# Kernel optimization log

Hardware: AMD Instinct MI355X
Metric: run time of the kernel (lower is better)

Reference implementation:

```python
import jax, jax.numpy as jnp
import numpy as np
import math

B, S, D, H = 2, 2048, 2048, 16
HD = D // H  # head_dim = 128
NEG = -9e15


def setup_inputs() -> dict:
    key = jax.random.key(0)
    k1, k2, k3 = jax.random.split(key, 3)
    x = jax.random.normal(k1, (B, S, D), dtype=jnp.float32)
    Wqkv = jax.random.normal(k2, (D, 3 * D), dtype=jnp.float32) * (1.0 / math.sqrt(D))
    bqkv = jnp.zeros((3 * D,), dtype=jnp.float32)
    Wo = jax.random.normal(k3, (D, D), dtype=jnp.float32) * (1.0 / math.sqrt(D))
    bo = jnp.zeros((D,), dtype=jnp.float32)
    return {"x": x, "Wqkv": Wqkv, "bqkv": bqkv, "Wo": Wo, "bo": bo}


def reference(x, Wqkv, bqkv, Wo, bo):
    b, s, d = x.shape
    # fused QKV projection
    qkv = x @ Wqkv + bqkv                       # [B,S,3D]
    qkv = qkv.reshape(b, s, H, 3 * HD)          # per-head interleaved q|k|v
    qkv = qkv.transpose(0, 2, 1, 3)             # [B,H,S,3*HD]
    q, k, v = jnp.split(qkv, 3, axis=-1)        # each [B,H,S,HD]
    scale = 1.0 / math.sqrt(HD)
    logits = jnp.einsum('bhqd,bhkd->bhqk', q, k) * scale  # [B,H,S,S]
    causal = jnp.tril(jnp.ones((s, s), dtype=bool))[None, None]
    logits = jnp.where(causal, logits, NEG)
    score = jax.nn.softmax(logits, axis=-1)
    attn = jnp.einsum('bhqk,bhkd->bhqd', score, v)         # [B,H,S,HD]
    attn = attn.transpose(0, 2, 1, 3).reshape(b, s, d)
    return attn @ Wo + bo
```

## Files before the change

### kernel.cpp

```cpp
#include <hip/hip_runtime.h>
#include <stdint.h>

#define DEV static __device__ __forceinline__

typedef _Float16 half8 __attribute__((ext_vector_type(8)));
typedef _Float16 half4 __attribute__((ext_vector_type(4)));
typedef float f32x4 __attribute__((ext_vector_type(4)));

constexpr int Bc = 2, Sc = 2048, Dc = 2048, Hc = 16, HDc = 128;
constexpr int D3c = 3 * Dc;
constexpr int Mc = Bc * Sc;

DEV void gl_lds16(const void* g, void* l) {
    __builtin_amdgcn_global_load_lds(
        (const __attribute__((address_space(1))) unsigned int*)g,
        (__attribute__((address_space(3))) unsigned int*)l,
        16, 0, 0);
}

__global__ __launch_bounds__(256) void cast_f16_kernel(
    const float* __restrict__ in, _Float16* __restrict__ out)
{
    int i = blockIdx.x * 256 + threadIdx.x;
    const float4* p = (const float4*)in;
    float4 a = p[i * 2], b = p[i * 2 + 1];
    half8 hv;
    hv[0] = (_Float16)a.x; hv[1] = (_Float16)a.y; hv[2] = (_Float16)a.z; hv[3] = (_Float16)a.w;
    hv[4] = (_Float16)b.x; hv[5] = (_Float16)b.y; hv[6] = (_Float16)b.z; hv[7] = (_Float16)b.w;
    *(half8*)(out + (size_t)i * 8) = hv;
}

__global__ __launch_bounds__(256) void transpose_cast_kernel(
    const float* __restrict__ in, _Float16* __restrict__ out, int R, int C)
{
    __shared__ float ls[64][65];
    const int t = threadIdx.x;
    const int r0 = blockIdx.y * 64, c0 = blockIdx.x * 64;
    const int rr = t >> 6, cc = t & 63;
#pragma unroll
    for (int i = 0; i < 16; ++i) {
        int r = i * 4 + rr;
        ls[r][cc] = in[(size_t)(r0 + r) * C + c0 + cc];
    }
    __syncthreads();
#pragma unroll
    for (int i = 0; i < 16; ++i) {
        int r = i * 4 + rr;
        out[(size_t)(c0 + r) * R + r0 + cc] = (_Float16)ls[cc][r];
    }
}

__global__ __launch_bounds__(256) void transpose_v_kernel(
    const uint16_t* __restrict__ qkv, uint16_t* __restrict__ vt)
{
    __shared__ uint32_t ls[64][65];
    const int t = threadIdx.x;
    const int s0 = blockIdx.x * 64, d0 = blockIdx.y * 64, bh = blockIdx.z;
    const int b = bh >> 4, h = bh & 15;
    const int rr = t >> 6, cc = t & 63;
#pragma unroll
    for (int i = 0; i < 16; ++i) {
        int r = i * 4 + rr;
        ls[r][cc] = qkv[(size_t)(b * Sc + s0 + r) * D3c + h * 384 + 256 + d0 + cc];
    }
    __syncthreads();
#pragma unroll
    for (int i = 0; i < 16; ++i) {
        int r = i * 4 + rr;
        vt[(size_t)(bh * HDc + d0 + r) * Sc + s0 + cc] = (uint16_t)ls[cc][r];
    }
}

template <int BF16OUT>
__global__ __launch_bounds__(256, 2) void gemm_bt_kernel(
    const _Float16* __restrict__ A, const _Float16* __restrict__ Bt,
    const float* __restrict__ bias, void* __restrict__ Cout,
    int M, int N, int K)
{
    __shared__ __align__(16) char smem[32768];
    char* sA = smem;
    char* sB = smem + 16384;
    const int t = threadIdx.x, w = t >> 6, lane = t & 63;
    const int quad = lane >> 4, l15 = lane & 15;
    const int wr = w >> 1, wc = w & 1;
    const int n0 = blockIdx.x * 128, m0 = blockIdx.y * 128;

    const f32x4 vzero = {0.f, 0.f, 0.f, 0.f};
    f32x4 acc[4][4];
#pragma unroll
    for (int i = 0; i < 4; ++i)
#pragma unroll
        for (int j = 0; j < 4; ++j) acc[i][j] = vzero;

    const int kiters = K >> 6;
    for (int kk = 0; kk < kiters; ++kk) {
#pragma unroll
        for (int i = 0; i < 4; ++i) {
            int c = i * 256 + t;
            int row = c >> 3, kbs = c & 7, kact = kbs ^ (row & 7);
            gl_lds16(A + (size_t)(m0 + row) * K + kk * 64 + kact * 8,
                     sA + (i * 256 + w * 64) * 16);
        }
#pragma unroll
        for (int i = 0; i < 4; ++i) {
            int c = i * 256 + t;
            int row = c >> 3, kbs = c & 7, kact = kbs ^ (row & 7);
            gl_lds16(Bt + (size_t)(n0 + row) * K + kk * 64 + kact * 8,
                     sB + (i * 256 + w * 64) * 16);
        }
        __syncthreads();
#pragma unroll
        for (int ks = 0; ks < 2; ++ks) {
            half8 af[4], bf[4];
#pragma unroll
            for (int mt = 0; mt < 4; ++mt) {
                int row = wr * 64 + mt * 16 + l15;
                int kact = (ks * 4 + quad) ^ (l15 & 7);
                af[mt] = *(const half8*)(sA + row * 128 + kact * 16);
            }
#pragma unroll
            for (int nt = 0; nt < 4; ++nt) {
                int row = wc * 64 + nt * 16 + l15;
                int kact = (ks * 4 + quad) ^ (l15 & 7);
                bf[nt] = *(const half8*)(sB + row * 128 + kact * 16);
            }
#pragma unroll
            for (int mt = 0; mt < 4; ++mt)
#pragma unroll
                for (int nt = 0; nt < 4; ++nt)
                    acc[mt][nt] = __builtin_amdgcn_mfma_f32_16x16x32_f16(
                        af[mt], bf[nt], acc[mt][nt], 0, 0, 0);
        }
        __syncthreads();
    }

#pragma unroll
    for (int nt = 0; nt < 4; ++nt) {
        int col = n0 + wc * 64 + nt * 16 + l15;
        float bv = bias[col];
#pragma unroll
        for (int mt = 0; mt < 4; ++mt)
#pragma unroll
            for (int r = 0; r < 4; ++r) {
                int row = m0 + wr * 64 + mt * 16 + quad * 4 + r;
                float v = acc[mt][nt][r] + bv;
                if (BF16OUT) ((_Float16*)Cout)[(size_t)row * N + col] = (_Float16)v;
                else         ((float*)Cout)[(size_t)row * N + col] = v;
            }
    }
}

__global__ __launch_bounds__(256, 4) void flash_kernel(
    const _Float16* __restrict__ qkv, const _Float16* __restrict__ vt,
    _Float16* __restrict__ attn)
{
    __shared__ __align__(16) char smem[32768];
    char* sK = smem;
    char* sV = smem + 16384;

    const int t = threadIdx.x, w = t >> 6, lane = t & 63;
    const int quad = lane >> 4, l15 = lane & 15;
    const int bh = blockIdx.x;
    const int qt = 31 - blockIdx.y;
    const int b = bh >> 4, h = bh & 15;
    const int q0 = qt * 64;
    const int qrow = q0 + w * 16 + l15;

    half8 qf[4];
#pragma unroll
    for (int ks = 0; ks < 4; ++ks) {
        const _Float16* p = qkv + (size_t)(b * Sc + qrow) * D3c +
                            h * 384 + ks * 32 + quad * 8;
        qf[ks] = *(const half8*)p;
    }

    const f32x4 vzero = {0.f, 0.f, 0.f, 0.f};
    f32x4 o[8];
#pragma unroll
    for (int dt = 0; dt < 8; ++dt) o[dt] = vzero;
    float m_st = -1e30f, l_st = 0.f;

    const float kScale = 0.08838834764831845f * 1.4426950408889634f;
    const int nkt = qt + 1;

    for (int kt = 0; kt < nkt; ++kt) {
#pragma unroll
        for (int i = 0; i < 4; ++i) {
            int c = i * 256 + t;
            int row = c >> 4, kbs = c & 15, kact = kbs ^ (row & 15);
            gl_lds16(qkv + (size_t)(b * Sc + kt * 64 + row) * D3c + h * 384 + 128 + kact * 8,
                     sK + (i * 256 + w * 64) * 16);
        }
#pragma unroll
        for (int i = 0; i < 4; ++i) {
            int c = i * 256 + t;
            int row = c >> 3, kbs = c & 7, kact = kbs ^ (row & 7);
            gl_lds16(vt + (size_t)(bh * HDc + row) * Sc + kt * 64 + kact * 8,
                     sV + (i * 256 + w * 64) * 16);
        }
        __syncthreads();

        f32x4 sf[4];
#pragma unroll
        for (int kb = 0; kb < 4; ++kb) sf[kb] = vzero;
#pragma unroll
        for (int ks = 0; ks < 4; ++ks) {
#pragma unroll
            for (int kb = 0; kb < 4; ++kb) {
                int row = kb * 16 + l15;
                int slot = (ks * 4 + quad) ^ l15;
                half8 kf = *(const half8*)(sK + row * 256 + slot * 16);
                sf[kb] = __builtin_amdgcn_mfma_f32_16x16x32_f16(kf, qf[ks], sf[kb], 0, 0, 0);
            }
        }

        const bool domask = (kt == qt);
        float rm = -1e30f;
#pragma unroll
        for (int kb = 0; kb < 4; ++kb)
#pragma unroll
            for (int r = 0; r < 4; ++r) {
                float v = sf[kb][r] * kScale;
                if (domask) {
                    int col = kt * 64 + kb * 16 + quad * 4 + r;
                    if (col > qrow) v = -1e30f;
                }
                sf[kb][r] = v;
                rm = fmaxf(rm, v);
            }
        rm = fmaxf(rm, __shfl_xor(rm, 16, 64));
        rm = fmaxf(rm, __shfl_xor(rm, 32, 64));
        float mn = fmaxf(m_st, rm);
        float alpha = __builtin_amdgcn_exp2f(m_st - mn);
        m_st = mn;

        half4 pb[4];
        float rs = 0.f;
#pragma unroll
        for (int kb = 0; kb < 4; ++kb)
#pragma unroll
            for (int r = 0; r < 4; ++r) {
                float p = __builtin_amdgcn_exp2f(sf[kb][r] - mn);
                rs += p;
                pb[kb][r] = (_Float16)p;
            }
        rs += __shfl_xor(rs, 16, 64);
        rs += __shfl_xor(rs, 32, 64);
        l_st = l_st * alpha + rs;

#pragma unroll
        for (int dt = 0; dt < 8; ++dt)
#pragma unroll
            for (int r = 0; r < 4; ++r) o[dt][r] *= alpha;

#pragma unroll
        for (int kb = 0; kb < 4; ++kb) {
#pragma unroll
            for (int dt = 0; dt < 8; ++dt) {
                int row = dt * 16 + l15;
                int slot = (kb * 2 + (quad >> 1)) ^ (l15 & 7);
                half4 vf = *(const half4*)(sV + row * 128 + slot * 16 + (quad & 1) * 8);
                o[dt] = __builtin_amdgcn_mfma_f32_16x16x16f16(vf, pb[kb], o[dt], 0, 0, 0);
            }
        }
        __syncthreads();
    }

    char* sO = smem;
    float linv = 1.0f / l_st;
#pragma unroll
    for (int dt = 0; dt < 8; ++dt) {
        half4 hv;
#pragma unroll
        for (int r = 0; r < 4; ++r) hv[r] = (_Float16)(o[dt][r] * linv);
        *(half4*)(sO + (w * 16 + l15) * 272 + (dt * 16 + quad * 4) * 2) = hv;
    }
    __syncthreads();
#pragma unroll
    for (int i = 0; i < 4; ++i) {
        int q = i * 16 + (t >> 4);
        int d = (t & 15) * 8;
        half8 hv = *(const half8*)(sO + q * 272 + d * 2);
        *(half8*)(attn + (size_t)(b * Sc + q0 + q) * Dc + h * HDc + d) = hv;
    }
}

extern "C" void kernel_launch(void* const* d_in, const int* in_sizes, int n_in,
                              void* d_out, int out_size, void* d_ws, size_t ws_size,
                              hipStream_t stream)
{
    (void)in_sizes; (void)n_in; (void)out_size; (void)ws_size;
    const float* x    = (const float*)d_in[0];
    const float* Wqkv = (const float*)d_in[1];
    const float* bqkv = (const float*)d_in[2];
    const float* Wo   = (const float*)d_in[3];
    const float* bo   = (const float*)d_in[4];
    float* out = (float*)d_out;

    _Float16* xb  = (_Float16*)d_ws;
    _Float16* wt1 = xb  + (size_t)Mc * Dc;
    _Float16* wt2 = wt1 + (size_t)D3c * Dc;
    _Float16* qkv = wt2 + (size_t)Dc * Dc;
    _Float16* vtg  = wt1;
    _Float16* attn = xb;

    cast_f16_kernel<<<Mc * Dc / 2048, 256, 0, stream>>>(x, xb);
    transpose_cast_kernel<<<dim3(D3c / 64, Dc / 64), 256, 0, stream>>>(Wqkv, wt1, Dc, D3c);
    transpose_cast_kernel<<<dim3(Dc / 64, Dc / 64), 256, 0, stream>>>(Wo, wt2, Dc, Dc);
    gemm_bt_kernel<1><<<dim3(D3c / 128, Mc / 128), 256, 0, stream>>>(
        xb, wt1, bqkv, qkv, Mc, D3c, Dc);
    transpose_v_kernel<<<dim3(Sc / 64, 2, Bc * Hc), 256, 0, stream>>>(
        (const uint16_t*)qkv, (uint16_t*)vtg);
    flash_kernel<<<dim3(Bc * Hc, 32), 256, 0, stream>>>(qkv, vtg, attn);
    gemm_bt_kernel<0><<<dim3(Dc / 128, Mc / 128), 256, 0, stream>>>(
        attn, wt2, bo, out, Mc, Dc, Dc);
}
```

Measured before the change: 383.7 us.

## Triple-buffer GEMM K-loop with async LDS prefetch and vectorize transpose kernels

The GEMM main loop moves from a single 64-wide K tile with two barriers per iteration to a three-stage ring of 32-wide K tiles. Each iteration prefetches two tiles ahead with direct global-to-LDS loads and waits through explicit vmcnt counts, so memory latency overlaps MFMA work. LDS grows to 48KB and launch bounds request 3 blocks per CU, which may reduce register headroom. The transpose kernels now use vectorized float4/8-element loads and stores with padded LDS rows to cut instruction count and bank conflicts.

Result: slower. 403.3 us (+5.1%).

```diff
diff --git a/kernel.cpp b/kernel.cpp
--- a/kernel.cpp
+++ b/kernel.cpp
@@ -6,6 +6,7 @@
 typedef _Float16 half8 __attribute__((ext_vector_type(8)));
 typedef _Float16 half4 __attribute__((ext_vector_type(4)));
 typedef float f32x4 __attribute__((ext_vector_type(4)));
+typedef uint16_t u16x8 __attribute__((ext_vector_type(8)));
 
 constexpr int Bc = 2, Sc = 2048, Dc = 2048, Hc = 16, HDc = 128;
 constexpr int D3c = 3 * Dc;
@@ -33,58 +34,80 @@
 __global__ __launch_bounds__(256) void transpose_cast_kernel(
     const float* __restrict__ in, _Float16* __restrict__ out, int R, int C)
 {
-    __shared__ float ls[64][65];
+    __shared__ float ls[64][68];
     const int t = threadIdx.x;
     const int r0 = blockIdx.y * 64, c0 = blockIdx.x * 64;
-    const int rr = t >> 6, cc = t & 63;
-#pragma unroll
-    for (int i = 0; i < 16; ++i) {
-        int r = i * 4 + rr;
-        ls[r][cc] = in[(size_t)(r0 + r) * C + c0 + cc];
+    {
+        const int rr = t >> 4, c4 = (t & 15) * 4;
+#pragma unroll
+        for (int p = 0; p < 4; ++p) {
+            int r = p * 16 + rr;
+            *(float4*)&ls[r][c4] = *(const float4*)&in[(size_t)(r0 + r) * C + c0 + c4];
+        }
     }
     __syncthreads();
-#pragma unroll
-    for (int i = 0; i < 16; ++i) {
-        int r = i * 4 + rr;
-        out[(size_t)(c0 + r) * R + r0 + cc] = (_Float16)ls[cc][r];
+    {
+        const int oc = t >> 3, sseg = (t & 7) * 8;
+#pragma unroll
+        for (int p = 0; p < 2; ++p) {
+            int c = p * 32 + oc;
+            half8 hv;
+#pragma unroll
+            for (int j = 0; j < 8; ++j) hv[j] = (_Float16)ls[sseg + j][c];
+            *(half8*)&out[(size_t)(c0 + c) * R + r0 + sseg] = hv;
+        }
     }
 }
 
 __global__ __launch_bounds__(256) void transpose_v_kernel(
     const uint16_t* __restrict__ qkv, uint16_t* __restrict__ vt)
 {
-    __shared__ uint32_t ls[64][65];
+    __shared__ uint16_t ls[64][72];
     const int t = threadIdx.x;
     const int s0 = blockIdx.x * 64, d0 = blockIdx.y * 64, bh = blockIdx.z;
     const int b = bh >> 4, h = bh & 15;
-    const int rr = t >> 6, cc = t & 63;
-#pragma unroll
-    for (int i = 0; i < 16; ++i) {
-        int r = i * 4 + rr;
-        ls[r][cc] = qkv[(size_t)(b * Sc + s0 + r) * D3c + h * 384 + 256 + d0 + cc];
+    {
+        const int sr = t >> 3, dc = (t & 7) * 8;
+#pragma unroll
+        for (int p = 0; p < 2; ++p) {
+            int s = p * 32 + sr;
+            *(u16x8*)&ls[s][dc] =
+                *(const u16x8*)&qkv[(size_t)(b * Sc + s0 + s) * D3c + h * 384 + 256 + d0 + dc];
+        }
     }
     __syncthreads();
-#pragma unroll
-    for (int i = 0; i < 16; ++i) {
-        int r = i * 4 + rr;
-        vt[(size_t)(bh * HDc + d0 + r) * Sc + s0 + cc] = (uint16_t)ls[cc][r];
+    {
+        const int od = t >> 3, ss = (t & 7) * 8;
+#pragma unroll
+        for (int p = 0; p < 2; ++p) {
+            int d = p * 32 + od;
+            u16x8 hv;
+#pragma unroll
+            for (int j = 0; j < 8; ++j) hv[j] = ls[ss + j][d];
+            *(u16x8*)&vt[(size_t)(bh * HDc + d0 + d) * Sc + s0 + ss] = hv;
+        }
     }
 }
 
 template <int BF16OUT>
-__global__ __launch_bounds__(256, 2) void gemm_bt_kernel(
+__global__ __launch_bounds__(256, 3) void gemm_bt_kernel(
     const _Float16* __restrict__ A, const _Float16* __restrict__ Bt,
     const float* __restrict__ bias, void* __restrict__ Cout,
     int M, int N, int K)
 {
-    __shared__ __align__(16) char smem[32768];
-    char* sA = smem;
-    char* sB = smem + 16384;
+    __shared__ __align__(16) char smem[49152];
     const int t = threadIdx.x, w = t >> 6, lane = t & 63;
     const int quad = lane >> 4, l15 = lane & 15;
     const int wr = w >> 1, wc = w & 1;
     const int n0 = blockIdx.x * 128, m0 = blockIdx.y * 128;
 
+    char* sA0 = smem;          char* sB0 = smem + 8192;
+    char* sA1 = smem + 16384;  char* sB1 = smem + 24576;
+    char* sA2 = smem + 32768;  char* sB2 = smem + 40960;
+    char *cA = sA0, *cB = sB0;
+    char *nA = sA1, *nB = sB1;
+    char *sA_ = sA2, *sB_ = sB2;
+
     const f32x4 vzero = {0.f, 0.f, 0.f, 0.f};
     f32x4 acc[4][4];
 #pragma unroll
@@ -92,46 +115,64 @@
 #pragma unroll
         for (int j = 0; j < 4; ++j) acc[i][j] = vzero;
 
-    const int kiters = K >> 6;
-    for (int kk = 0; kk < kiters; ++kk) {
-#pragma unroll
-        for (int i = 0; i < 4; ++i) {
-            int c = i * 256 + t;
-            int row = c >> 3, kbs = c & 7, kact = kbs ^ (row & 7);
-            gl_lds16(A + (size_t)(m0 + row) * K + kk * 64 + kact * 8,
-                     sA + (i * 256 + w * 64) * 16);
-        }
-#pragma unroll
-        for (int i = 0; i < 4; ++i) {
-            int c = i * 256 + t;
-            int row = c >> 3, kbs = c & 7, kact = kbs ^ (row & 7);
-            gl_lds16(Bt + (size_t)(n0 + row) * K + kk * 64 + kact * 8,
-                     sB + (i * 256 + w * 64) * 16);
-        }
-        __syncthreads();
-#pragma unroll
-        for (int ks = 0; ks < 2; ++ks) {
-            half8 af[4], bf[4];
-#pragma unroll
-            for (int mt = 0; mt < 4; ++mt) {
-                int row = wr * 64 + mt * 16 + l15;
-                int kact = (ks * 4 + quad) ^ (l15 & 7);
-                af[mt] = *(const half8*)(sA + row * 128 + kact * 16);
-            }
-#pragma unroll
-            for (int nt = 0; nt < 4; ++nt) {
-                int row = wc * 64 + nt * 16 + l15;
-                int kact = (ks * 4 + quad) ^ (l15 & 7);
-                bf[nt] = *(const half8*)(sB + row * 128 + kact * 16);
-            }
-#pragma unroll
-            for (int mt = 0; mt < 4; ++mt)
-#pragma unroll
-                for (int nt = 0; nt < 4; ++nt)
-                    acc[mt][nt] = __builtin_amdgcn_mfma_f32_16x16x32_f16(
-                        af[mt], bf[nt], acc[mt][nt], 0, 0, 0);
-        }
-        __syncthreads();
+    const int rS = t >> 2;
+    const int ciS = (t & 3) ^ (rS & 3);
+    const _Float16* ga0 = A  + (size_t)(m0 + rS) * K + ciS * 8;
+    const _Float16* ga1 = A  + (size_t)(m0 + 64 + rS) * K + ciS * 8;
+    const _Float16* gb0 = Bt + (size_t)(n0 + rS) * K + ciS * 8;
+    const _Float16* gb1 = Bt + (size_t)(n0 + 64 + rS) * K + ciS * 8;
+    const int ldsOff0 = (w * 64) * 16, ldsOff1 = (256 + w * 64) * 16;
+
+    int offA[4], offB[4];
+#pragma unroll
+    for (int mt = 0; mt < 4; ++mt)
+        offA[mt] = (wr * 64 + mt * 16 + l15) * 64 + ((quad ^ (l15 & 3)) * 16);
+#pragma unroll
+    for (int nt = 0; nt < 4; ++nt)
+        offB[nt] = (wc * 64 + nt * 16 + l15) * 64 + ((quad ^ (l15 & 3)) * 16);
+
+    const int kiters = K >> 5;
+
+    gl_lds16(ga0, sA0 + ldsOff0); gl_lds16(ga1, sA0 + ldsOff1);
+    gl_lds16(gb0, sB0 + ldsOff0); gl_lds16(gb1, sB0 + ldsOff1);
+    ga0 += 32; ga1 += 32; gb0 += 32; gb1 += 32;
+    gl_lds16(ga0, sA1 + ldsOff0); gl_lds16(ga1, sA1 + ldsOff1);
+    gl_lds16(gb0, sB1 + ldsOff0); gl_lds16(gb1, sB1 + ldsOff1);
+    ga0 += 32; ga1 += 32; gb0 += 32; gb1 += 32;
+    asm volatile("s_waitcnt vmcnt(4)" ::: "memory");
+    __builtin_amdgcn_s_barrier();
+    __builtin_amdgcn_sched_barrier(0);
+
+    for (int kt = 0; kt < kiters; ++kt) {
+        half8 af[4], bf[4];
+#pragma unroll
+        for (int mt = 0; mt < 4; ++mt) af[mt] = *(const half8*)(cA + offA[mt]);
+#pragma unroll
+        for (int nt = 0; nt < 4; ++nt) bf[nt] = *(const half8*)(cB + offB[nt]);
+
+        const bool do_stage = (kt + 2 < kiters);
+        if (do_stage) {
+            gl_lds16(ga0, sA_ + ldsOff0); gl_lds16(ga1, sA_ + ldsOff1);
+            gl_lds16(gb0, sB_ + ldsOff0); gl_lds16(gb1, sB_ + ldsOff1);
+            ga0 += 32; ga1 += 32; gb0 += 32; gb1 += 32;
+        }
+
+#pragma unroll
+        for (int mt = 0; mt < 4; ++mt)
+#pragma unroll
+            for (int nt = 0; nt < 4; ++nt)
+                acc[mt][nt] = __builtin_amdgcn_mfma_f32_16x16x32_f16(
+                    af[mt], bf[nt], acc[mt][nt], 0, 0, 0);
+
+        if (kt + 1 < kiters) {
+            if (do_stage) asm volatile("s_waitcnt vmcnt(4) lgkmcnt(0)" ::: "memory");
+            else          asm volatile("s_waitcnt vmcnt(0) lgkmcnt(0)" ::: "memory");
+            __builtin_amdgcn_s_barrier();
+            __builtin_amdgcn_sched_barrier(0);
+            char* tp;
+            tp = cA; cA = nA; nA = sA_; sA_ = tp;
+            tp = cB; cB = nB; nB = sB_; sB_ = tp;
+        }
     }
 
 #pragma unroll
```

## Double-buffer GEMM LDS tiles and vectorize transpose kernels with XOR swizzle

Applied to the files above, without the earlier changes.

The GEMM now uses two LDS buffers, issuing the global-to-LDS loads for the next K tile before computing on the current one. This overlaps memory latency with MFMA work and removes one barrier per iteration, at the cost of doubling LDS to 64KB, which may limit occupancy. The transpose_cast and V-transpose kernels now move data with 16-byte vector loads and stores through an XOR-swizzled LDS tile instead of scalar accesses with padding.

After: 379.3 us. Within noise of the previous version (-1.1%).

```diff
diff --git a/kernel.cpp b/kernel.cpp
--- a/kernel.cpp
+++ b/kernel.cpp
@@ -6,6 +6,7 @@
 typedef _Float16 half8 __attribute__((ext_vector_type(8)));
 typedef _Float16 half4 __attribute__((ext_vector_type(4)));
 typedef float f32x4 __attribute__((ext_vector_type(4)));
+typedef uint16_t u16x8 __attribute__((ext_vector_type(8)));
 
 constexpr int Bc = 2, Sc = 2048, Dc = 2048, Hc = 16, HDc = 128;
 constexpr int D3c = 3 * Dc;
@@ -33,41 +34,69 @@
 __global__ __launch_bounds__(256) void transpose_cast_kernel(
     const float* __restrict__ in, _Float16* __restrict__ out, int R, int C)
 {
-    __shared__ float ls[64][65];
+    __shared__ float ls[64][64];
     const int t = threadIdx.x;
     const int r0 = blockIdx.y * 64, c0 = blockIdx.x * 64;
-    const int rr = t >> 6, cc = t & 63;
-#pragma unroll
-    for (int i = 0; i < 16; ++i) {
-        int r = i * 4 + rr;
-        ls[r][cc] = in[(size_t)(r0 + r) * C + c0 + cc];
+    {
+        const int rr = t >> 4, lc = t & 15;
+#pragma unroll
+        for (int p = 0; p < 4; ++p) {
+            int r = p * 16 + rr;
+            int pc = lc ^ ((r >> 3) & 7);
+            *(float4*)&ls[r][pc * 4] =
+                *(const float4*)&in[(size_t)(r0 + r) * C + c0 + lc * 4];
+        }
     }
     __syncthreads();
-#pragma unroll
-    for (int i = 0; i < 16; ++i) {
-        int r = i * 4 + rr;
-        out[(size_t)(c0 + r) * R + r0 + cc] = (_Float16)ls[cc][r];
+    {
+        const int oc = t >> 3, ss = (t & 7) * 8;
+#pragma unroll
+        for (int p = 0; p < 2; ++p) {
+            int c = p * 32 + oc;
+            int lc = c >> 2, wi = c & 3;
+            half8 hv;
+#pragma unroll
+            for (int j = 0; j < 8; ++j) {
+                int r = ss + j;
+                hv[j] = (_Float16)ls[r][(lc ^ ((r >> 3) & 7)) * 4 + wi];
+            }
+            *(half8*)&out[(size_t)(c0 + c) * R + r0 + ss] = hv;
+        }
     }
 }
 
 __global__ __launch_bounds__(256) void transpose_v_kernel(
     const uint16_t* __restrict__ qkv, uint16_t* __restrict__ vt)
 {
-    __shared__ uint32_t ls[64][65];
+    __shared__ uint16_t ls[64][64];
     const int t = threadIdx.x;
     const int s0 = blockIdx.x * 64, d0 = blockIdx.y * 64, bh = blockIdx.z;
     const int b = bh >> 4, h = bh & 15;
-    const int rr = t >> 6, cc = t & 63;
-#pragma unroll
-    for (int i = 0; i < 16; ++i) {
-        int r = i * 4 + rr;
-        ls[r][cc] = qkv[(size_t)(b * Sc + s0 + r) * D3c + h * 384 + 256 + d0 + cc];
+    {
+        const int sr = t >> 3, lc = t & 7;
+#pragma unroll
+        for (int p = 0; p < 2; ++p) {
+            int s = p * 32 + sr;
+            int pc = lc ^ ((s >> 3) & 7);
+            *(u16x8*)&ls[s][pc * 8] =
+                *(const u16x8*)&qkv[(size_t)(b * Sc + s0 + s) * D3c + h * 384 + 256 + d0 + lc * 8];
+        }
     }
     __syncthreads();
-#pragma unroll
-    for (int i = 0; i < 16; ++i) {
-        int r = i * 4 + rr;
-        vt[(size_t)(bh * HDc + d0 + r) * Sc + s0 + cc] = (uint16_t)ls[cc][r];
+    {
+        const int od = t >> 3, ss = (t & 7) * 8;
+#pragma unroll
+        for (int p = 0; p < 2; ++p) {
+            int d = p * 32 + od;
+            int lc = d >> 3, wi = d & 7;
+            u16x8 hv;
+#pragma unroll
+            for (int j = 0; j < 8; ++j) {
+                int s = ss + j;
+                hv[j] = ls[s][(lc ^ ((s >> 3) & 7)) * 8 + wi];
+            }
+            *(u16x8*)&vt[(size_t)(bh * HDc + d0 + d) * Sc + s0 + ss] = hv;
+        }
     }
 }
 
@@ -77,14 +106,15 @@
     const float* __restrict__ bias, void* __restrict__ Cout,
     int M, int N, int K)
 {
-    __shared__ __align__(16) char smem[32768];
-    char* sA = smem;
-    char* sB = smem + 16384;
+    __shared__ __align__(16) char smem[65536];
     const int t = threadIdx.x, w = t >> 6, lane = t & 63;
     const int quad = lane >> 4, l15 = lane & 15;
     const int wr = w >> 1, wc = w & 1;
     const int n0 = blockIdx.x * 128, m0 = blockIdx.y * 128;
 
+    char *cA = smem,         *cB = smem + 16384;
+    char *nA = smem + 32768, *nB = smem + 49152;
+
     const f32x4 vzero = {0.f, 0.f, 0.f, 0.f};
     f32x4 acc[4][4];
 #pragma unroll
@@ -92,23 +122,31 @@
 #pragma unroll
         for (int j = 0; j < 4; ++j) acc[i][j] = vzero;
 
-    const int kiters = K >> 6;
-    for (int kk = 0; kk < kiters; ++kk) {
+    auto stage = [&](char* dA, char* dB, int kk) {
 #pragma unroll
         for (int i = 0; i < 4; ++i) {
             int c = i * 256 + t;
             int row = c >> 3, kbs = c & 7, kact = kbs ^ (row & 7);
             gl_lds16(A + (size_t)(m0 + row) * K + kk * 64 + kact * 8,
-                     sA + (i * 256 + w * 64) * 16);
+                     dA + (i * 256 + w * 64) * 16);
         }
 #pragma unroll
         for (int i = 0; i < 4; ++i) {
             int c = i * 256 + t;
             int row = c >> 3, kbs = c & 7, kact = kbs ^ (row & 7);
             gl_lds16(Bt + (size_t)(n0 + row) * K + kk * 64 + kact * 8,
-                     sB + (i * 256 + w * 64) * 16);
-        }
-        __syncthreads();
+                     dB + (i * 256 + w * 64) * 16);
+        }
+    };
+
+    const int kiters = K >> 6;
+    stage(cA, cB, 0);
+    __syncthreads();
+
+    for (int kt = 0; kt < kiters; ++kt) {
+        const bool more = (kt + 1 < kiters);
+        if (more) stage(nA, nB, kt + 1);
+
 #pragma unroll
         for (int ks = 0; ks < 2; ++ks) {
             half8 af[4], bf[4];
@@ -116,13 +154,13 @@
             for (int mt = 0; mt < 4; ++mt) {
                 int row = wr * 64 + mt * 16 + l15;
                 int kact = (ks * 4 + quad) ^ (l15 & 7);
-                af[mt] = *(const half8*)(sA + row * 128 + kact * 16);
+                af[mt] = *(const half8*)(cA + row * 128 + kact * 16);
             }
 #pragma unroll
             for (int nt = 0; nt < 4; ++nt) {
                 int row = wc * 64 + nt * 16 + l15;
                 int kact = (ks * 4 + quad) ^ (l15 & 7);
-                bf[nt] = *(const half8*)(sB + row * 128 + kact * 16);
+                bf[nt] = *(const half8*)(cB + row * 128 + kact * 16);
             }
 #pragma unroll
             for (int mt = 0; mt < 4; ++mt)
@@ -131,7 +169,13 @@
                     acc[mt][nt] = __builtin_amdgcn_mfma_f32_16x16x32_f16(
                         af[mt], bf[nt], acc[mt][nt], 0, 0, 0);
         }
-        __syncthreads();
+
+        if (more) {
+            __syncthreads();
+            char* tp;
+            tp = cA; cA = nA; nA = tp;
+            tp = cB; cB = nB; nB = tp;
+        }
     }
 
 #pragma unroll
```
